# Performance work log

Hardware: AMD Instinct MI355X
Metric: run time of the kernel (lower is better)

Reference implementation:

```python
import jax, jax.numpy as jnp
import numpy as np

E = 1024
M = 6
GH = 256
FR = 16  # FiLM bottleneck r = max(16, E//64)


def setup_inputs() -> dict:
    key = jax.random.key(0)
    ks = jax.random.split(key, 32)
    n = lambda k, shape, std=0.02: jax.random.normal(k, shape, dtype=jnp.float32) * std
    inp = {
        "x": jax.random.normal(ks[0], (4, 2048, E), dtype=jnp.float32),
        # gate MLP E->GH->M
        "gw1": n(ks[1], (E, GH)), "gb1": jnp.zeros((GH,), jnp.float32),
        "gw2": n(ks[2], (GH, M)), "gb2": jnp.zeros((M,), jnp.float32),
        "ebias": jnp.zeros((M,), jnp.float32),
        "pm_alpha": jnp.float32(0.5),
        # expert 0: DoubleMLP E->2E->E
        "dfc_w": n(ks[3], (E, 2 * E)), "dfc_b": jnp.zeros((2 * E,), jnp.float32),
        "dproj_w": n(ks[4], (2 * E, E)), "dproj_b": jnp.zeros((E,), jnp.float32),
        # expert 1: SingleMLP E->E->E
        "sfc_w": n(ks[5], (E, E)), "sfc_b": jnp.zeros((E,), jnp.float32),
        "sproj_w": n(ks[6], (E, E)), "sproj_b": jnp.zeros((E,), jnp.float32),
        # expert 2: rank-2 perceptron
        "p2_w": n(ks[7], (2, E)), "p2_v": n(ks[8], (2, E)),
        "p2_alpha": jnp.ones((2,), jnp.float32), "p2_b": jnp.zeros((2,), jnp.float32),
        "p2_bias": jnp.zeros((E,), jnp.float32),
        # expert 3: rank-4 perceptron
        "p4_w": n(ks[9], (4, E)), "p4_v": n(ks[10], (4, E)),
        "p4_alpha": jnp.ones((4,), jnp.float32), "p4_b": jnp.zeros((4,), jnp.float32),
        "p4_bias": jnp.zeros((E,), jnp.float32),
        # expert 4: ReGLU1D
        "rg_u": n(ks[11], (E,)), "rg_a": jnp.ones((E,), jnp.float32),
        "rg_b": jnp.zeros((1,), jnp.float32), "rg_bias": jnp.zeros((E,), jnp.float32),
        # expert 5: FiLM E->FR->2E
        "fl_dw": n(ks[12], (E, FR)), "fl_db": jnp.zeros((FR,), jnp.float32),
        "fl_uw": n(ks[13], (FR, 2 * E)), "fl_ub": jnp.zeros((2 * E,), jnp.float32),
    }
    return inp


def _gelu(x):
    return jax.nn.gelu(x, approximate=False)  # torch nn.GELU default (erf)


def _rank_n(x, w, v, alpha, b, biasvec):
    # y = biasvec + sum_i alpha_i * gelu(<w_i,x> + b_i) * v_i
    s = jnp.einsum("bse,ne->bsn", x, w) + b
    g = _gelu(s)
    return jnp.einsum("bsn,ne->bse", alpha * g, v) + biasvec


def reference(x, gw1, gb1, gw2, gb2, ebias, pm_alpha,
              dfc_w, dfc_b, dproj_w, dproj_b,
              sfc_w, sfc_b, sproj_w, sproj_b,
              p2_w, p2_v, p2_alpha, p2_b, p2_bias,
              p4_w, p4_v, p4_alpha, p4_b, p4_bias,
              rg_u, rg_a, rg_b, rg_bias,
              fl_dw, fl_db, fl_uw, fl_ub):
    # gate logits [B,S,M]; tau=1.0
    gl = _gelu(x @ gw1 + gb1) @ gw2 + gb2 + ebias
    pi = jax.nn.softmax(gl, axis=-1)
    # top_k=1 sparse weights: mask to top-1 then renormalize
    _, topi = jax.lax.top_k(pi, 1)
    mask = jax.nn.one_hot(topi[..., 0], M, dtype=pi.dtype)
    w = pi * mask
    w = w / (jnp.sum(w, axis=-1, keepdims=True) + 1e-9)

    # experts (dropout = identity in eval)
    o0 = _gelu(x @ dfc_w + dfc_b) @ dproj_w + dproj_b            # DoubleMLP
    o1 = _gelu(x @ sfc_w + sfc_b) @ sproj_w + sproj_b            # SingleMLP
    o2 = _rank_n(x, p2_w, p2_v, p2_alpha, p2_b, p2_bias)          # perc2
    o3 = _rank_n(x, p4_w, p4_v, p4_alpha, p4_b, p4_bias)          # perc4
    s = x @ rg_u + rg_b[0]                                        # ReGLU1D
    o4 = jax.nn.sigmoid(s)[..., None] * (x * rg_a) + rg_bias
    t = _gelu(x @ fl_dw + fl_db)                                  # FiLM
    gb = t @ fl_uw + fl_ub
    gamma, beta = jnp.split(gb, 2, axis=-1)
    o5 = gamma * x + beta

    all_out = jnp.stack([o0, o1, o2, o3, o4, o5], axis=-1)        # [B,S,E,M]
    mixed = jnp.sum(all_out * w[..., None, :], axis=-1)
    return pm_alpha * mixed
```

## Files before the change

### kernel.cpp

```cpp
#include <hip/hip_runtime.h>
#include <math.h>


#define E 1024
#define GH 256
#define NEXP 6
#define NTOK 8192
#define NCH 24

typedef __attribute__((ext_vector_type(8))) short bf16x8;
typedef __attribute__((ext_vector_type(4))) float f32x4;

__device__ __forceinline__ float gelu_erf(float v) {
    return 0.5f * v * (1.0f + erff(v * 0.70710678118654752440f));
}

__device__ __forceinline__ unsigned short f2bf(float f) {
    union { float f; unsigned u; } c; c.f = f;
    unsigned u = c.u;
    u += 0x7fffu + ((u >> 16) & 1u);
    return (unsigned short)(u >> 16);
}

__device__ __forceinline__ float bf2f(unsigned short h) {
    union { unsigned u; float f; } c; c.u = ((unsigned)h) << 16;
    return c.f;
}

__device__ __forceinline__ int ldso(int row, int q) {
    return row * 32 + ((q ^ ((row >> 1) & 3)) << 3);
}

__device__ __forceinline__ void glds16(const void* g, void* l) {
    __builtin_amdgcn_global_load_lds(
        (const __attribute__((address_space(1))) void*)g,
        (__attribute__((address_space(3))) void*)l, 16, 0, 0);
}

__global__ __launch_bounds__(256)
void prep_kernel(const float* __restrict__ x, unsigned short* __restrict__ xh,
                 unsigned short* __restrict__ xl,
                 const float* __restrict__ gw1, unsigned short* __restrict__ w1cat,
                 const float* __restrict__ p2_w, const float* __restrict__ p4_w,
                 const float* __restrict__ rg_u, const float* __restrict__ fl_dw,
                 unsigned short* __restrict__ w1cheap,
                 const float* __restrict__ dfc_w, unsigned short* __restrict__ dfc_wt,
                 const float* __restrict__ dproj_w, unsigned short* __restrict__ dpj_wt,
                 const float* __restrict__ sfc_w, unsigned short* __restrict__ sfc_wt,
                 const float* __restrict__ sproj_w, unsigned short* __restrict__ spj_wt) {
    __shared__ float tile[32][33];
    const int tid = threadIdx.x;
    const int tx = tid & 31, ty = tid >> 5;
    int b = blockIdx.x;
    if (b < 2048) {
        const int n4 = NTOK * E / 4;
        for (int i = b * 256 + tid; i < n4; i += 2048 * 256) {
            float4 v = reinterpret_cast<const float4*>(x)[i];
            ushort4 h, l;
            h.x = f2bf(v.x); l.x = f2bf(v.x - bf2f(h.x));
            h.y = f2bf(v.y); l.y = f2bf(v.y - bf2f(h.y));
            h.z = f2bf(v.z); l.z = f2bf(v.z - bf2f(h.z));
            h.w = f2bf(v.w); l.w = f2bf(v.w - bf2f(h.w));
            reinterpret_cast<ushort4*>(xh)[i] = h;
            reinterpret_cast<ushort4*>(xl)[i] = l;
        }
        return;
    }
    b -= 2048;
    if (b < 256) {
        const int c0 = (b & 7) * 32, r0 = (b >> 3) * 32;
#pragma unroll
        for (int i = 0; i < 4; ++i)
            tile[ty + i * 8][tx] = gw1[(size_t)(r0 + ty + i * 8) * GH + c0 + tx];
        __syncthreads();
#pragma unroll
        for (int i = 0; i < 4; ++i) {
            float v = tile[tx][ty + i * 8];
            unsigned short h = f2bf(v);
            size_t row = (size_t)(c0 + ty + i * 8) * 2048;
            w1cat[row + r0 + tx] = h;
            w1cat[row + 1024 + r0 + tx] = f2bf(v - bf2f(h));
        }
        return;
    }
    b -= 256;
    if (b < 64) {
        const int r = b;
        const int k4 = tid * 4;
        float4 v = {0.f, 0.f, 0.f, 0.f};
        if (r < 2)       v = *reinterpret_cast<const float4*>(&p2_w[r * E + k4]);
        else if (r < 6)  v = *reinterpret_cast<const float4*>(&p4_w[(r - 2) * E + k4]);
        else if (r == 6) v = *reinterpret_cast<const float4*>(&rg_u[k4]);
        else if (r < 23) {
            const int j = r - 7;
            v.x = fl_dw[(k4 + 0) * 16 + j];
            v.y = fl_dw[(k4 + 1) * 16 + j];
            v.z = fl_dw[(k4 + 2) * 16 + j];
            v.w = fl_dw[(k4 + 3) * 16 + j];
        }
        ushort4 h, l;
        h.x = f2bf(v.x); l.x = f2bf(v.x - bf2f(h.x));
        h.y = f2bf(v.y); l.y = f2bf(v.y - bf2f(h.y));
        h.z = f2bf(v.z); l.z = f2bf(v.z - bf2f(h.z));
        h.w = f2bf(v.w); l.w = f2bf(v.w - bf2f(h.w));
        *reinterpret_cast<ushort4*>(&w1cheap[r * 2048 + k4]) = h;
        *reinterpret_cast<ushort4*>(&w1cheap[r * 2048 + 1024 + k4]) = l;
        return;
    }
    b -= 64;
    const float* src; unsigned short* dst; int R, C, nbx;
    if (b < 2048)      { src = dfc_w;   dst = dfc_wt; R = 1024; C = 2048; nbx = 64; }
    else if (b < 4096) { src = dproj_w; dst = dpj_wt; R = 2048; C = 1024; nbx = 32; b -= 2048; }
    else if (b < 5120) { src = sfc_w;   dst = sfc_wt; R = 1024; C = 1024; nbx = 32; b -= 4096; }
    else               { src = sproj_w; dst = spj_wt; R = 1024; C = 1024; nbx = 32; b -= 5120; }
    const int c0 = (b % nbx) * 32, r0 = (b / nbx) * 32;
#pragma unroll
    for (int i = 0; i < 4; ++i)
        tile[ty + i * 8][tx] = src[(size_t)(r0 + ty + i * 8) * C + c0 + tx];
    __syncthreads();
#pragma unroll
    for (int i = 0; i < 4; ++i)
        dst[(size_t)(c0 + ty + i * 8) * R + r0 + tx] = f2bf(tile[tx][ty + i * 8]);
}

__global__ __launch_bounds__(256)
void gate_partial_kernel(const unsigned short* __restrict__ xh,
                         const unsigned short* __restrict__ xl,
                         const unsigned short* __restrict__ w1cat,
                         const unsigned short* __restrict__ w1cheap,
                         float* __restrict__ hp,
                         float* __restrict__ cdot) {
    __shared__ __align__(16) unsigned short As[2][128 * 32];
    __shared__ __align__(16) unsigned short Bs[2][128 * 32];
    const int tid = threadIdx.x;
    const int bid = blockIdx.x;
    const int xcd = bid & 7, slot = bid >> 3;
    const int nx = slot & 1;
    const int strip = xcd * 32 + (slot >> 1);
    const int m = strip >> 2, c2 = strip & 3;
    const int z = c2 & 1, h = c2 >> 1;
    const int t0 = m * 128, n0 = nx * 128;
    const unsigned short* A = z ? xl : xh;
    float* hpz = hp + (size_t)c2 * ((size_t)NTOK * GH);
    float* cd  = cdot + (size_t)c2 * ((size_t)NTOK * NCH);

    const int lane = tid & 63, wv = tid >> 6;
    const int wr = wv >> 1, wc = wv & 1;
    const int lm = lane & 15, q = lane >> 4;
    const int r0 = tid >> 2, gsl = tid & 3;
    const int g = gsl ^ ((r0 >> 1) & 3);
    const int lbase = wv * 512;

    const unsigned short* pa0 = A + (size_t)(t0 + r0) * E + g * 8;
    const unsigned short* pa1 = A + (size_t)(t0 + 64 + r0) * E + g * 8;
    const unsigned short* pb0 = w1cat + (size_t)(n0 + r0) * 2048 + h * 1024 + g * 8;
    const unsigned short* pb1 = w1cat + (size_t)(n0 + 64 + r0) * 2048 + h * 1024 + g * 8;
    const unsigned short* pcw = w1cheap + (size_t)(nx * 16 + lm) * 2048 + h * 1024 + q * 8;

    f32x4 acc[4][4];
#pragma unroll
    for (int s = 0; s < 4; ++s)
#pragma unroll
        for (int t = 0; t < 4; ++t) acc[s][t] = (f32x4){0.f, 0.f, 0.f, 0.f};
    f32x4 accC[2];
    accC[0] = (f32x4){0.f, 0.f, 0.f, 0.f};
    accC[1] = (f32x4){0.f, 0.f, 0.f, 0.f};

    glds16(pa0, &As[0][lbase]);
    glds16(pa1, &As[0][2048 + lbase]);
    glds16(pb0, &Bs[0][lbase]);
    glds16(pb1, &Bs[0][2048 + lbase]);
    bf16x8 cfv = *(const bf16x8*)pcw;

    int cur = 0;
    for (int k0 = 0;; k0 += 32) {
        __syncthreads();
        const int kn = k0 + 32;
        bf16x8 cfn;
        if (kn < 1024) {
            glds16(pa0 + kn, &As[cur ^ 1][lbase]);
            glds16(pa1 + kn, &As[cur ^ 1][2048 + lbase]);
            glds16(pb0 + kn, &Bs[cur ^ 1][lbase]);
            glds16(pb1 + kn, &Bs[cur ^ 1][2048 + lbase]);
            cfn = *(const bf16x8*)(pcw + kn);
        }
        bf16x8 af[4], bfr[4];
#pragma unroll
        for (int s = 0; s < 4; ++s) af[s] = *(const bf16x8*)&As[cur][ldso(wr * 64 + s * 16 + lm, q)];
#pragma unroll
        for (int t = 0; t < 4; ++t) bfr[t] = *(const bf16x8*)&Bs[cur][ldso(wc * 64 + t * 16 + lm, q)];
#pragma unroll
        for (int s = 0; s < 4; ++s)
#pragma unroll
            for (int t = 0; t < 4; ++t)
                acc[s][t] = __builtin_amdgcn_mfma_f32_16x16x32_bf16(af[s], bfr[t], acc[s][t], 0, 0, 0);
        {
            bf16x8 ac0 = wc ? af[2] : af[0];
            bf16x8 ac1 = wc ? af[3] : af[1];
            accC[0] = __builtin_amdgcn_mfma_f32_16x16x32_bf16(ac0, cfv, accC[0], 0, 0, 0);
            accC[1] = __builtin_amdgcn_mfma_f32_16x16x32_bf16(ac1, cfv, accC[1], 0, 0, 0);
        }
        if (kn >= 1024) break;
        cfv = cfn; cur ^= 1;
    }
#pragma unroll
    for (int s = 0; s < 4; ++s)
#pragma unroll
        for (int t = 0; t < 4; ++t)
#pragma unroll
            for (int rg = 0; rg < 4; ++rg) {
                int rl = wr * 64 + s * 16 + q * 4 + rg;
                int c  = wc * 64 + t * 16 + lm;
                hpz[(size_t)(t0 + rl) * GH + n0 + c] = acc[s][t][rg];
            }
    const int cc = nx * 16 + lm;
    if (cc < NCH) {
#pragma unroll
        for (int i = 0; i < 2; ++i)
#pragma unroll
            for (int rg = 0; rg < 4; ++rg) {
                int rl = wr * 64 + wc * 32 + i * 16 + q * 4 + rg;
                cd[(size_t)(t0 + rl) * NCH + cc] = accC[i][rg];
            }
    }
}

__global__ __launch_bounds__(256)
void gate_finalize_kernel(const float* __restrict__ hp,
                          const float* __restrict__ gb1, const float* __restrict__ gw2,
                          const float* __restrict__ gb2, const float* __restrict__ ebias,
                          const float* __restrict__ pm_alpha,
                          const float* __restrict__ cdot,
                          const float* __restrict__ p2_alpha, const float* __restrict__ p2_b,
                          const float* __restrict__ p4_alpha, const float* __restrict__ p4_b,
                          const float* __restrict__ rg_b, const float* __restrict__ fl_db,
                          float* __restrict__ scale, int* __restrict__ counts,
                          int* __restrict__ tlist, int* __restrict__ eid,
                          float* __restrict__ gvec) {
    __shared__ float hs[32][264];
    __shared__ float g2s[GH * NEXP];
    __shared__ int tokexp[32];
    const int tid = threadIdx.x;
    const int t0 = blockIdx.x * 32;
    const size_t HPS = (size_t)NTOK * GH;
    for (int i = tid; i < GH * NEXP; i += 256) g2s[i] = gw2[i];
#pragma unroll
    for (int i = 0; i < 8; ++i) {
        int f4 = i * 256 + tid;
        int row = f4 >> 6, c4 = (f4 & 63) * 4;
        size_t base = (size_t)(t0 + row) * GH + c4;
        float4 a = *reinterpret_cast<const float4*>(&hp[base]);
        float4 b = *reinterpret_cast<const float4*>(&hp[HPS + base]);
        float4 c = *reinterpret_cast<const float4*>(&hp[2 * HPS + base]);
        float4 d = *reinterpret_cast<const float4*>(&hp[3 * HPS + base]);
        float4 o;
        o.x = gelu_erf(a.x + b.x + c.x + d.x + gb1[c4 + 0]);
        o.y = gelu_erf(a.y + b.y + c.y + d.y + gb1[c4 + 1]);
        o.z = gelu_erf(a.z + b.z + c.z + d.z + gb1[c4 + 2]);
        o.w = gelu_erf(a.w + b.w + c.w + d.w + gb1[c4 + 3]);
        *reinterpret_cast<float4*>(&hs[row][c4]) = o;
    }
    __syncthreads();
    const int t = tid >> 3, j = tid & 7;
    float p[NEXP] = {0.f, 0.f, 0.f, 0.f, 0.f, 0.f};
#pragma unroll 8
    for (int kk = 0; kk < 32; ++kk) {
        int k = j + kk * 8;
        float hv = hs[t][k];
        const float* gr = &g2s[k * NEXP];
#pragma unroll
        for (int m = 0; m < NEXP; ++m) p[m] += hv * gr[m];
    }
#pragma unroll
    for (int m = 0; m < NEXP; ++m) {
        p[m] += __shfl_xor(p[m], 4, 64);
        p[m] += __shfl_xor(p[m], 2, 64);
        p[m] += __shfl_xor(p[m], 1, 64);
    }
    if (j == 0) {
        float L[NEXP];
#pragma unroll
        for (int m = 0; m < NEXP; ++m) L[m] = p[m] + gb2[m] + ebias[m];
        float mx = L[0]; int am = 0;
#pragma unroll
        for (int m = 1; m < NEXP; ++m) { if (L[m] > mx) { mx = L[m]; am = m; } }
        float S = 0.f;
#pragma unroll
        for (int m = 0; m < NEXP; ++m) S += expf(L[m] - mx);
        float pt = 1.f / S;
        scale[t0 + t] = pm_alpha[0] * (pt / (pt + 1e-9f));
        eid[t0 + t] = am;
        tokexp[t] = am;
    }
    __syncthreads();
    if (tid < NEXP) {
        const int e = tid;
        int cnt = 0;
#pragma unroll
        for (int i = 0; i < 32; ++i) cnt += (tokexp[i] == e);
        if (cnt) {
            int base = atomicAdd(&counts[e], cnt);
            int pos = 0;
#pragma unroll
            for (int i = 0; i < 32; ++i)
                if (tokexp[i] == e) tlist[e * NTOK + base + (pos++)] = t0 + i;
        }
    }
    const size_t CDS = (size_t)NTOK * NCH;
    for (int i = tid; i < 32 * NCH; i += 256) {
        const int tt = i / NCH, slot = i - tt * NCH;
        const int tok = t0 + tt;
        size_t idx = (size_t)tok * NCH + slot;
        float s = cdot[idx] + cdot[CDS + idx] + cdot[2 * CDS + idx] + cdot[3 * CDS + idx];
        float val;
        if (slot < 2)       val = p2_alpha[slot] * gelu_erf(s + p2_b[slot]);
        else if (slot < 6)  val = p4_alpha[slot - 2] * gelu_erf(s + p4_b[slot - 2]);
        else if (slot == 6) val = 1.f / (1.f + expf(-(s + rg_b[0])));
        else if (slot < 23) val = gelu_erf(s + fl_db[slot - 7]);
        else                val = 0.f;
        gvec[(size_t)tok * NCH + slot] = val;
    }
}

__global__ __launch_bounds__(256)
void moe_gemm1_kernel(const unsigned short* __restrict__ xh,
                      const unsigned short* __restrict__ B0, const unsigned short* __restrict__ B1,
                      const float* __restrict__ bias0, const float* __restrict__ bias1,
                      const int* __restrict__ counts, const int* __restrict__ tlist,
                      unsigned short* __restrict__ H0, unsigned short* __restrict__ H1) {
    __shared__ __align__(16) unsigned short As[2][64 * 32];
    __shared__ __align__(16) unsigned short Bs[2][64 * 32];
    __shared__ int toks[64];
    const int tid = threadIdx.x;
    const int bid = blockIdx.x;
    const int xcd = bid & 7, slot = bid >> 3;
    const int nx = slot & 31;
    const int strip = xcd + 8 * (slot >> 5);
    const int z = strip & 1;
    const int N = z ? 1024 : 2048;
    const int cnt = counts[z];
    const int i0 = (strip >> 1) * 64;
    const int n0 = nx * 64;
    if (i0 >= cnt || n0 >= N) return;
    const unsigned short* Bz = z ? B1 : B0;
    const float* bias = z ? bias1 : bias0;

    if (tid < 64) toks[tid] = tlist[z * NTOK + min(i0 + tid, cnt - 1)];
    __syncthreads();

    const int lane = tid & 63, wv = tid >> 6;
    const int wm = (wv & 1) * 32, wn = (wv >> 1) * 32;
    const int lm = lane & 15, q = lane >> 4;
    const int r0 = tid >> 2, gsl = tid & 3;
    const int g = gsl ^ ((r0 >> 1) & 3);
    const int lbase = wv * 512;

    const unsigned short* pa = xh + (size_t)toks[r0] * E + g * 8;
    const unsigned short* pb = Bz + (size_t)(n0 + r0) * E + g * 8;

    f32x4 acc[2][2];
#pragma unroll
    for (int s = 0; s < 2; ++s)
#pragma unroll
        for (int t = 0; t < 2; ++t) acc[s][t] = (f32x4){0.f, 0.f, 0.f, 0.f};

    glds16(pa, &As[0][lbase]);
    glds16(pb, &Bs[0][lbase]);

    int cur = 0;
    for (int k0 = 0;; k0 += 32) {
        __syncthreads();
        const int kn = k0 + 32;
        if (kn < E) {
            glds16(pa + kn, &As[cur ^ 1][lbase]);
            glds16(pb + kn, &Bs[cur ^ 1][lbase]);
        }
        bf16x8 af[2], bfr[2];
#pragma unroll
        for (int s = 0; s < 2; ++s) af[s] = *(const bf16x8*)&As[cur][ldso(wm + s * 16 + lm, q)];
#pragma unroll
        for (int t = 0; t < 2; ++t) bfr[t] = *(const bf16x8*)&Bs[cur][ldso(wn + t * 16 + lm, q)];
#pragma unroll
        for (int s = 0; s < 2; ++s)
#pragma unroll
            for (int t = 0; t < 2; ++t)
                acc[s][t] = __builtin_amdgcn_mfma_f32_16x16x32_bf16(af[s], bfr[t], acc[s][t], 0, 0, 0);
        if (kn >= E) break;
        cur ^= 1;
    }
    unsigned short* Hz = z ? H1 : H0;
#pragma unroll
    for (int s = 0; s < 2; ++s)
#pragma unroll
        for (int t = 0; t < 2; ++t)
#pragma unroll
            for (int rg = 0; rg < 4; ++rg) {
                int rl = wm + s * 16 + q * 4 + rg;
                int gc = n0 + wn + t * 16 + lm;
                float v = acc[s][t][rg] + bias[gc];
                Hz[(size_t)(i0 + rl) * N + gc] = f2bf(gelu_erf(v));
            }
}

__global__ __launch_bounds__(256)
void gemm2_cheap_kernel(const unsigned short* __restrict__ h1, const unsigned short* __restrict__ h2,
                        const unsigned short* __restrict__ dpj, const unsigned short* __restrict__ spj,
                        const float* __restrict__ dproj_b, const float* __restrict__ sproj_b,
                        const int* __restrict__ counts, const int* __restrict__ tlist,
                        const float* __restrict__ scale,
                        const float* __restrict__ x, const float* __restrict__ gvec,
                        const float* __restrict__ p2_v, const float* __restrict__ p2_bias,
                        const float* __restrict__ p4_v, const float* __restrict__ p4_bias,
                        const float* __restrict__ rg_a, const float* __restrict__ rg_bias,
                        const float* __restrict__ fl_uw, const float* __restrict__ fl_ub,
                        float* __restrict__ out) {
    __shared__ __align__(16) char smem[2 * 64 * 32 * 2 * 2 + 64 * 4];
    const int tid = threadIdx.x;
    const int bb = blockIdx.x;
    const int lane = tid & 63;

    if (bb < 1024) {
        const int xcd = bb & 7, slot = bb >> 3;
        const int nx = slot & 15;
        const int strip = xcd + 8 * (slot >> 4);
        const int z = strip & 1;
        const int i0 = (strip >> 1) * 64;
        const int n0 = nx * 64;
        const int K = z ? 1024 : 2048;
        const int cnt = counts[z];
        if (i0 >= cnt) return;
        const int rows = min(64, cnt - i0);
        const unsigned short* Az = z ? h2 : h1;
        const unsigned short* Bz = z ? spj : dpj;
        const float* bias = z ? sproj_b : dproj_b;

        unsigned short (*As)[64 * 32] = (unsigned short (*)[64 * 32])smem;
        unsigned short (*Bs)[64 * 32] = (unsigned short (*)[64 * 32])(smem + 2 * 64 * 32 * 2);
        int* toks = (int*)(smem + 2 * 64 * 32 * 2 * 2);
        if (tid < 64) toks[tid] = tlist[z * NTOK + min(i0 + tid, cnt - 1)];
        __syncthreads();

        const int wv = tid >> 6;
        const int wm = (wv & 1) * 32, wn = (wv >> 1) * 32;
        const int lm = lane & 15, q = lane >> 4;
        const int r0 = tid >> 2, gsl = tid & 3;
        const int g = gsl ^ ((r0 >> 1) & 3);
        const int lbase = wv * 512;

        const unsigned short* pa = Az + (size_t)(i0 + r0) * K + g * 8;
        const unsigned short* pb = Bz + (size_t)(n0 + r0) * K + g * 8;

        f32x4 acc[2][2];
#pragma unroll
        for (int s = 0; s < 2; ++s)
#pragma unroll
            for (int t = 0; t < 2; ++t) acc[s][t] = (f32x4){0.f, 0.f, 0.f, 0.f};

        glds16(pa, &As[0][lbase]);
        glds16(pb, &Bs[0][lbase]);

        int cur = 0;
        for (int k0 = 0;; k0 += 32) {
            __syncthreads();
            const int kn = k0 + 32;
            if (kn < K) {
                glds16(pa + kn, &As[cur ^ 1][lbase]);
                glds16(pb + kn, &Bs[cur ^ 1][lbase]);
            }
            bf16x8 af[2], bfr[2];
#pragma unroll
            for (int s = 0; s < 2; ++s) af[s] = *(const bf16x8*)&As[cur][ldso(wm + s * 16 + lm, q)];
#pragma unroll
            for (int t = 0; t < 2; ++t) bfr[t] = *(const bf16x8*)&Bs[cur][ldso(wn + t * 16 + lm, q)];
#pragma unroll
            for (int s = 0; s < 2; ++s)
#pragma unroll
                for (int t = 0; t < 2; ++t)
                    acc[s][t] = __builtin_amdgcn_mfma_f32_16x16x32_bf16(af[s], bfr[t], acc[s][t], 0, 0, 0);
            if (kn >= K) break;
            cur ^= 1;
        }
#pragma unroll
        for (int s = 0; s < 2; ++s)
#pragma unroll
            for (int t = 0; t < 2; ++t)
#pragma unroll
                for (int rg = 0; rg < 4; ++rg) {
                    int rl = wm + s * 16 + q * 4 + rg;
                    if (rl < rows) {
                        int gc = n0 + wn + t * 16 + lm;
                        int tok = toks[rl];
                        out[(size_t)tok * E + gc] = scale[tok] * (acc[s][t][rg] + bias[gc]);
                    }
                }
        return;
    }

    int* stoks = (int*)smem;
    float* ssc = (float*)(smem + 32);
    float (*sgv)[17] = (float (*)[17])(smem + 64);
    const int k4 = tid * 4;
    for (int s = bb - 1024; s < 4096; s += 2048) {
        const int e = 2 + (s & 3);
        const int ti = s >> 2;
        const int cnt = counts[e];
        const int i0 = ti * 8;
        if (i0 >= cnt) continue;
        const int nt = min(8, cnt - i0);
        __syncthreads();
        if (tid < 128) {
            const int tt = tid >> 4, sl = tid & 15;
            const int tk = tlist[e * NTOK + min(i0 + tt, cnt - 1)];
            if (sl == 0) { stoks[tt] = tk; ssc[tt] = scale[tk]; }
            const int base = (e == 2) ? 0 : (e == 3) ? 2 : (e == 4) ? 6 : 7;
            const int ng   = (e == 2) ? 2 : (e == 3) ? 4 : (e == 4) ? 1 : 16;
            if (sl < ng) sgv[tt][sl] = gvec[(size_t)tk * NCH + base + sl];
        }
        __syncthreads();
        if (e == 2) {
            const float4 b0 = *reinterpret_cast<const float4*>(&p2_bias[k4]);
            const float4 v0 = *reinterpret_cast<const float4*>(&p2_v[k4]);
            const float4 v1 = *reinterpret_cast<const float4*>(&p2_v[E + k4]);
#pragma unroll
            for (int tt = 0; tt < 8; ++tt) {
                if (tt < nt) {
                    const float g0 = sgv[tt][0], g1 = sgv[tt][1], sc = ssc[tt];
                    float4 o;
                    o.x = (b0.x + g0 * v0.x + g1 * v1.x) * sc;
                    o.y = (b0.y + g0 * v0.y + g1 * v1.y) * sc;
                    o.z = (b0.z + g0 * v0.z + g1 * v1.z) * sc;
                    o.w = (b0.w + g0 * v0.w + g1 * v1.w) * sc;
                    *reinterpret_cast<float4*>(&out[(size_t)stoks[tt] * E + k4]) = o;
                }
            }
        } else if (e == 3) {
            const float4 b0 = *reinterpret_cast<const float4*>(&p4_bias[k4]);
            float4 vv[4];
#pragma unroll
            for (int j = 0; j < 4; ++j)
                vv[j] = *reinterpret_cast<const float4*>(&p4_v[j * E + k4]);
#pragma unroll
            for (int tt = 0; tt < 8; ++tt) {
                if (tt < nt) {
                    float4 o = b0;
#pragma unroll
                    for (int j = 0; j < 4; ++j) {
                        const float gj = sgv[tt][j];
                        o.x += gj * vv[j].x; o.y += gj * vv[j].y;
                        o.z += gj * vv[j].z; o.w += gj * vv[j].w;
                    }
                    const float sc = ssc[tt];
                    o.x *= sc; o.y *= sc; o.z *= sc; o.w *= sc;
                    *reinterpret_cast<float4*>(&out[(size_t)stoks[tt] * E + k4]) = o;
                }
            }
        } else if (e == 4) {
            const float4 av = *reinterpret_cast<const float4*>(&rg_a[k4]);
            const float4 bv = *reinterpret_cast<const float4*>(&rg_bias[k4]);
#pragma unroll
            for (int tt = 0; tt < 8; ++tt) {
                if (tt < nt) {
                    const float sg = sgv[tt][0], sc = ssc[tt];
                    const float4 xv = *reinterpret_cast<const float4*>(&x[(size_t)stoks[tt] * E + k4]);
                    float4 o;
                    o.x = (sg * xv.x * av.x + bv.x) * sc;
                    o.y = (sg * xv.y * av.y + bv.y) * sc;
                    o.z = (sg * xv.z * av.z + bv.z) * sc;
                    o.w = (sg * xv.w * av.w + bv.w) * sc;
                    *reinterpret_cast<float4*>(&out[(size_t)stoks[tt] * E + k4]) = o;
                }
            }
        } else {
            float4 ga[8], be[8];
            const float4 g0 = *reinterpret_cast<const float4*>(&fl_ub[k4]);
            const float4 b0 = *reinterpret_cast<const float4*>(&fl_ub[E + k4]);
#pragma unroll
            for (int tt = 0; tt < 8; ++tt) { ga[tt] = g0; be[tt] = b0; }
#pragma unroll
            for (int j = 0; j < 16; ++j) {
                const float4 ug = *reinterpret_cast<const float4*>(&fl_uw[(size_t)j * 2 * E + k4]);
                const float4 ub = *reinterpret_cast<const float4*>(&fl_uw[(size_t)j * 2 * E + E + k4]);
#pragma unroll
                for (int tt = 0; tt < 8; ++tt) {
                    const float tj = sgv[tt][j];
                    ga[tt].x += tj * ug.x; ga[tt].y += tj * ug.y;
                    ga[tt].z += tj * ug.z; ga[tt].w += tj * ug.w;
                    be[tt].x += tj * ub.x; be[tt].y += tj * ub.y;
                    be[tt].z += tj * ub.z; be[tt].w += tj * ub.w;
                }
            }
#pragma unroll
            for (int tt = 0; tt < 8; ++tt) {
                if (tt < nt) {
                    const float sc = ssc[tt];
                    const float4 xv = *reinterpret_cast<const float4*>(&x[(size_t)stoks[tt] * E + k4]);
                    float4 o;
                    o.x = (ga[tt].x * xv.x + be[tt].x) * sc;
                    o.y = (ga[tt].y * xv.y + be[tt].y) * sc;
                    o.z = (ga[tt].z * xv.z + be[tt].z) * sc;
                    o.w = (ga[tt].w * xv.w + be[tt].w) * sc;
                    *reinterpret_cast<float4*>(&out[(size_t)stoks[tt] * E + k4]) = o;
                }
            }
        }
    }
}

extern "C" void kernel_launch(void* const* d_in, const int* in_sizes, int n_in,
                              void* d_out, int out_size, void* d_ws, size_t ws_size,
                              hipStream_t stream) {
    const float* x        = (const float*)d_in[0];
    const float* gw1      = (const float*)d_in[1];
    const float* gb1      = (const float*)d_in[2];
    const float* gw2      = (const float*)d_in[3];
    const float* gb2      = (const float*)d_in[4];
    const float* ebias    = (const float*)d_in[5];
    const float* pm_alpha = (const float*)d_in[6];
    const float* dfc_w    = (const float*)d_in[7];
    const float* dfc_b    = (const float*)d_in[8];
    const float* dproj_w  = (const float*)d_in[9];
    const float* dproj_b  = (const float*)d_in[10];
    const float* sfc_w    = (const float*)d_in[11];
    const float* sfc_b    = (const float*)d_in[12];
    const float* sproj_w  = (const float*)d_in[13];
    const float* sproj_b  = (const float*)d_in[14];
    const float* p2_w     = (const float*)d_in[15];
    const float* p2_v     = (const float*)d_in[16];
    const float* p2_alpha = (const float*)d_in[17];
    const float* p2_b     = (const float*)d_in[18];
    const float* p2_bias  = (const float*)d_in[19];
    const float* p4_w     = (const float*)d_in[20];
    const float* p4_v     = (const float*)d_in[21];
    const float* p4_alpha = (const float*)d_in[22];
    const float* p4_b     = (const float*)d_in[23];
    const float* p4_bias  = (const float*)d_in[24];
    const float* rg_u     = (const float*)d_in[25];
    const float* rg_a     = (const float*)d_in[26];
    const float* rg_b     = (const float*)d_in[27];
    const float* rg_bias  = (const float*)d_in[28];
    const float* fl_dw    = (const float*)d_in[29];
    const float* fl_db    = (const float*)d_in[30];
    const float* fl_uw    = (const float*)d_in[31];
    const float* fl_ub    = (const float*)d_in[32];
    float* out = (float*)d_out;

    char* ws = (char*)d_ws;
    size_t off = 0;
    int*            counts = (int*)(ws + off);            off += 256;
    float*          scale  = (float*)(ws + off);          off += (size_t)NTOK * 4;
    int*            tlist  = (int*)(ws + off);            off += (size_t)NEXP * NTOK * 4;
    int*            eid    = (int*)(ws + off);            off += (size_t)NTOK * 4;
    float*          gvec   = (float*)(ws + off);          off += (size_t)NTOK * NCH * 4;
    float*          cdot   = (float*)(ws + off);          off += (size_t)4 * NTOK * NCH * 4;
    unsigned short* w1cheap= (unsigned short*)(ws + off); off += (size_t)64 * 2048 * 2;
    unsigned short* w1cat  = (unsigned short*)(ws + off); off += (size_t)GH * 2048 * 2;
    unsigned short* dfc_wt = (unsigned short*)(ws + off); off += (size_t)2048 * 1024 * 2;
    unsigned short* dpj_wt = (unsigned short*)(ws + off); off += (size_t)1024 * 2048 * 2;
    unsigned short* sfc_wt = (unsigned short*)(ws + off); off += (size_t)1024 * 1024 * 2;
    unsigned short* spj_wt = (unsigned short*)(ws + off); off += (size_t)1024 * 1024 * 2;
    unsigned short* x_hi   = (unsigned short*)(ws + off); off += (size_t)NTOK * E * 2;
    char* U = ws + off;
    unsigned short* x_lo = (unsigned short*)U;
    unsigned short* h1   = (unsigned short*)U;
    unsigned short* h2   = (unsigned short*)(U + (size_t)16 * 1024 * 1024);
    float* hp = out;

    hipMemsetAsync(counts, 0, 256, stream);
    prep_kernel<<<8512, 256, 0, stream>>>(x, x_hi, x_lo, gw1, w1cat,
                                          p2_w, p4_w, rg_u, fl_dw, w1cheap,
                                          dfc_w, dfc_wt, dproj_w, dpj_wt,
                                          sfc_w, sfc_wt, sproj_w, spj_wt);
    gate_partial_kernel<<<512, 256, 0, stream>>>(
        x_hi, x_lo, w1cat, w1cheap, hp, cdot);
    gate_finalize_kernel<<<NTOK / 32, 256, 0, stream>>>(
        hp, gb1, gw2, gb2, ebias, pm_alpha, cdot,
        p2_alpha, p2_b, p4_alpha, p4_b, rg_b, fl_db,
        scale, counts, tlist, eid, gvec);
    moe_gemm1_kernel<<<2048, 256, 0, stream>>>(
        x_hi, dfc_wt, sfc_wt, dfc_b, sfc_b, counts, tlist, h1, h2);
    gemm2_cheap_kernel<<<1024 + 2048, 256, 0, stream>>>(
        h1, h2, dpj_wt, spj_wt, dproj_b, sproj_b, counts, tlist, scale,
        x, gvec,
        p2_v, p2_bias, p4_v, p4_bias,
        rg_a, rg_bias, fl_uw, fl_ub, out);
    (void)in_sizes; (void)n_in; (void)out_size; (void)ws_size;
}
```

Measured before the change: 294.0 us.

## Fuse cheap experts into gemm1 launch and double K-step per iteration

The cheap-expert blocks (perceptrons, ReGLU, FiLM) now ride alongside the first MoE GEMM instead of the second, and the second GEMM becomes its own kernel. All bf16 GEMM loops (gate, gemm1, gemm2) now stage 64-wide K tiles per barrier instead of 32, halving the number of syncs. The FiLM path is split into two halves of four tokens to reduce register pressure. The larger LDS footprint may lower occupancy.

```diff
diff --git a/kernel.cpp b/kernel.cpp
--- a/kernel.cpp
+++ b/kernel.cpp
@@ -130,8 +130,8 @@
                          const unsigned short* __restrict__ w1cheap,
                          float* __restrict__ hp,
                          float* __restrict__ cdot) {
-    __shared__ __align__(16) unsigned short As[2][128 * 32];
-    __shared__ __align__(16) unsigned short Bs[2][128 * 32];
+    __shared__ __align__(16) unsigned short As[2][128 * 64];
+    __shared__ __align__(16) unsigned short Bs[2][128 * 64];
     const int tid = threadIdx.x;
     const int bid = blockIdx.x;
     const int xcd = bid & 7, slot = bid >> 3;
@@ -168,40 +168,53 @@
 
     glds16(pa0, &As[0][lbase]);
     glds16(pa1, &As[0][2048 + lbase]);
+    glds16(pa0 + 32, &As[0][4096 + lbase]);
+    glds16(pa1 + 32, &As[0][4096 + 2048 + lbase]);
     glds16(pb0, &Bs[0][lbase]);
     glds16(pb1, &Bs[0][2048 + lbase]);
-    bf16x8 cfv = *(const bf16x8*)pcw;
+    glds16(pb0 + 32, &Bs[0][4096 + lbase]);
+    glds16(pb1 + 32, &Bs[0][4096 + 2048 + lbase]);
+    bf16x8 cf0 = *(const bf16x8*)pcw;
+    bf16x8 cf1 = *(const bf16x8*)(pcw + 32);
 
     int cur = 0;
-    for (int k0 = 0;; k0 += 32) {
+    for (int k0 = 0;; k0 += 64) {
         __syncthreads();
-        const int kn = k0 + 32;
-        bf16x8 cfn;
+        const int kn = k0 + 64;
+        bf16x8 cf0n, cf1n;
         if (kn < 1024) {
             glds16(pa0 + kn, &As[cur ^ 1][lbase]);
             glds16(pa1 + kn, &As[cur ^ 1][2048 + lbase]);
+            glds16(pa0 + kn + 32, &As[cur ^ 1][4096 + lbase]);
+            glds16(pa1 + kn + 32, &As[cur ^ 1][4096 + 2048 + lbase]);
             glds16(pb0 + kn, &Bs[cur ^ 1][lbase]);
             glds16(pb1 + kn, &Bs[cur ^ 1][2048 + lbase]);
-            cfn = *(const bf16x8*)(pcw + kn);
-        }
-        bf16x8 af[4], bfr[4];
-#pragma unroll
-        for (int s = 0; s < 4; ++s) af[s] = *(const bf16x8*)&As[cur][ldso(wr * 64 + s * 16 + lm, q)];
-#pragma unroll
-        for (int t = 0; t < 4; ++t) bfr[t] = *(const bf16x8*)&Bs[cur][ldso(wc * 64 + t * 16 + lm, q)];
-#pragma unroll
-        for (int s = 0; s < 4; ++s)
-#pragma unroll
-            for (int t = 0; t < 4; ++t)
-                acc[s][t] = __builtin_amdgcn_mfma_f32_16x16x32_bf16(af[s], bfr[t], acc[s][t], 0, 0, 0);
-        {
+            glds16(pb0 + kn + 32, &Bs[cur ^ 1][4096 + lbase]);
+            glds16(pb1 + kn + 32, &Bs[cur ^ 1][4096 + 2048 + lbase]);
+            cf0n = *(const bf16x8*)(pcw + kn);
+            cf1n = *(const bf16x8*)(pcw + kn + 32);
+        }
+#pragma unroll
+        for (int sub = 0; sub < 2; ++sub) {
+            const int off = sub * 4096;
+            bf16x8 af[4], bfr[4];
+#pragma unroll
+            for (int s = 0; s < 4; ++s) af[s] = *(const bf16x8*)&As[cur][off + ldso(wr * 64 + s * 16 + lm, q)];
+#pragma unroll
+            for (int t = 0; t < 4; ++t) bfr[t] = *(const bf16x8*)&Bs[cur][off + ldso(wc * 64 + t * 16 + lm, q)];
+#pragma unroll
+            for (int s = 0; s < 4; ++s)
+#pragma unroll
+                for (int t = 0; t < 4; ++t)
+                    acc[s][t] = __builtin_amdgcn_mfma_f32_16x16x32_bf16(af[s], bfr[t], acc[s][t], 0, 0, 0);
+            bf16x8 cf = sub ? cf1 : cf0;
             bf16x8 ac0 = wc ? af[2] : af[0];
             bf16x8 ac1 = wc ? af[3] : af[1];
-            accC[0] = __builtin_amdgcn_mfma_f32_16x16x32_bf16(ac0, cfv, accC[0], 0, 0, 0);
-            accC[1] = __builtin_amdgcn_mfma_f32_16x16x32_bf16(ac1, cfv, accC[1], 0, 0, 0);
+            accC[0] = __builtin_amdgcn_mfma_f32_16x16x32_bf16(ac0, cf, accC[0], 0, 0, 0);
+            accC[1] = __builtin_amdgcn_mfma_f32_16x16x32_bf16(ac1, cf, accC[1], 0, 0, 0);
         }
         if (kn >= 1024) break;
-        cfv = cfn; cur ^= 1;
+        cf0 = cf0n; cf1 = cf1n; cur ^= 1;
     }
 #pragma unroll
     for (int s = 0; s < 4; ++s)
@@ -323,120 +336,39 @@
 }
 
 __global__ __launch_bounds__(256)
-void moe_gemm1_kernel(const unsigned short* __restrict__ xh,
-                      const unsigned short* __restrict__ B0, const unsigned short* __restrict__ B1,
-                      const float* __restrict__ bias0, const float* __restrict__ bias1,
-                      const int* __restrict__ counts, const int* __restrict__ tlist,
-                      unsigned short* __restrict__ H0, unsigned short* __restrict__ H1) {
-    __shared__ __align__(16) unsigned short As[2][64 * 32];
-    __shared__ __align__(16) unsigned short Bs[2][64 * 32];
-    __shared__ int toks[64];
-    const int tid = threadIdx.x;
-    const int bid = blockIdx.x;
-    const int xcd = bid & 7, slot = bid >> 3;
-    const int nx = slot & 31;
-    const int strip = xcd + 8 * (slot >> 5);
-    const int z = strip & 1;
-    const int N = z ? 1024 : 2048;
-    const int cnt = counts[z];
-    const int i0 = (strip >> 1) * 64;
-    const int n0 = nx * 64;
-    if (i0 >= cnt || n0 >= N) return;
-    const unsigned short* Bz = z ? B1 : B0;
-    const float* bias = z ? bias1 : bias0;
-
-    if (tid < 64) toks[tid] = tlist[z * NTOK + min(i0 + tid, cnt - 1)];
-    __syncthreads();
-
-    const int lane = tid & 63, wv = tid >> 6;
-    const int wm = (wv & 1) * 32, wn = (wv >> 1) * 32;
-    const int lm = lane & 15, q = lane >> 4;
-    const int r0 = tid >> 2, gsl = tid & 3;
-    const int g = gsl ^ ((r0 >> 1) & 3);
-    const int lbase = wv * 512;
-
-    const unsigned short* pa = xh + (size_t)toks[r0] * E + g * 8;
-    const unsigned short* pb = Bz + (size_t)(n0 + r0) * E + g * 8;
-
-    f32x4 acc[2][2];
-#pragma unroll
-    for (int s = 0; s < 2; ++s)
-#pragma unroll
-        for (int t = 0; t < 2; ++t) acc[s][t] = (f32x4){0.f, 0.f, 0.f, 0.f};
-
-    glds16(pa, &As[0][lbase]);
-    glds16(pb, &Bs[0][lbase]);
-
-    int cur = 0;
-    for (int k0 = 0;; k0 += 32) {
-        __syncthreads();
-        const int kn = k0 + 32;
-        if (kn < E) {
-            glds16(pa + kn, &As[cur ^ 1][lbase]);
-            glds16(pb + kn, &Bs[cur ^ 1][lbase]);
-        }
-        bf16x8 af[2], bfr[2];
-#pragma unroll
-        for (int s = 0; s < 2; ++s) af[s] = *(const bf16x8*)&As[cur][ldso(wm + s * 16 + lm, q)];
-#pragma unroll
-        for (int t = 0; t < 2; ++t) bfr[t] = *(const bf16x8*)&Bs[cur][ldso(wn + t * 16 + lm, q)];
-#pragma unroll
-        for (int s = 0; s < 2; ++s)
-#pragma unroll
-            for (int t = 0; t < 2; ++t)
-                acc[s][t] = __builtin_amdgcn_mfma_f32_16x16x32_bf16(af[s], bfr[t], acc[s][t], 0, 0, 0);
-        if (kn >= E) break;
-        cur ^= 1;
-    }
-    unsigned short* Hz = z ? H1 : H0;
-#pragma unroll
-    for (int s = 0; s < 2; ++s)
-#pragma unroll
-        for (int t = 0; t < 2; ++t)
-#pragma unroll
-            for (int rg = 0; rg < 4; ++rg) {
-                int rl = wm + s * 16 + q * 4 + rg;
-                int gc = n0 + wn + t * 16 + lm;
-                float v = acc[s][t][rg] + bias[gc];
-                Hz[(size_t)(i0 + rl) * N + gc] = f2bf(gelu_erf(v));
-            }
-}
-
-__global__ __launch_bounds__(256)
-void gemm2_cheap_kernel(const unsigned short* __restrict__ h1, const unsigned short* __restrict__ h2,
-                        const unsigned short* __restrict__ dpj, const unsigned short* __restrict__ spj,
-                        const float* __restrict__ dproj_b, const float* __restrict__ sproj_b,
+void gemm1_cheap_kernel(const unsigned short* __restrict__ xh,
+                        const unsigned short* __restrict__ B0, const unsigned short* __restrict__ B1,
+                        const float* __restrict__ bias0, const float* __restrict__ bias1,
                         const int* __restrict__ counts, const int* __restrict__ tlist,
-                        const float* __restrict__ scale,
-                        const float* __restrict__ x, const float* __restrict__ gvec,
+                        unsigned short* __restrict__ H0, unsigned short* __restrict__ H1,
+                        const float* __restrict__ scale, const float* __restrict__ x,
+                        const float* __restrict__ gvec,
                         const float* __restrict__ p2_v, const float* __restrict__ p2_bias,
                         const float* __restrict__ p4_v, const float* __restrict__ p4_bias,
                         const float* __restrict__ rg_a, const float* __restrict__ rg_bias,
                         const float* __restrict__ fl_uw, const float* __restrict__ fl_ub,
                         float* __restrict__ out) {
-    __shared__ __align__(16) char smem[2 * 64 * 32 * 2 * 2 + 64 * 4];
+    __shared__ __align__(16) char smem[2 * 64 * 64 * 2 * 2 + 64 * 4];
     const int tid = threadIdx.x;
     const int bb = blockIdx.x;
     const int lane = tid & 63;
 
-    if (bb < 1024) {
+    if (bb < 2048) {
         const int xcd = bb & 7, slot = bb >> 3;
-        const int nx = slot & 15;
-        const int strip = xcd + 8 * (slot >> 4);
+        const int nx = slot & 31;
+        const int strip = xcd + 8 * (slot >> 5);
         const int z = strip & 1;
+        const int N = z ? 1024 : 2048;
+        const int cnt = counts[z];
         const int i0 = (strip >> 1) * 64;
         const int n0 = nx * 64;
-        const int K = z ? 1024 : 2048;
-        const int cnt = counts[z];
-        if (i0 >= cnt) return;
-        const int rows = min(64, cnt - i0);
-        const unsigned short* Az = z ? h2 : h1;
-        const unsigned short* Bz = z ? spj : dpj;
-        const float* bias = z ? sproj_b : dproj_b;
-
-        unsigned short (*As)[64 * 32] = (unsigned short (*)[64 * 32])smem;
-        unsigned short (*Bs)[64 * 32] = (unsigned short (*)[64 * 32])(smem + 2 * 64 * 32 * 2);
-        int* toks = (int*)(smem + 2 * 64 * 32 * 2 * 2);
+        if (i0 >= cnt || n0 >= N) return;
+        const unsigned short* Bz = z ? B1 : B0;
+        const float* bias = z ? bias1 : bias0;
+
+        unsigned short (*As)[64 * 64] = (unsigned short (*)[64 * 64])smem;
+        unsigned short (*Bs)[64 * 64] = (unsigned short (*)[64 * 64])(smem + 2 * 64 * 64 * 2);
+        int* toks = (int*)(smem + 2 * 64 * 64 * 2 * 2);
         if (tid < 64) toks[tid] = tlist[z * NTOK + min(i0 + tid, cnt - 1)];
         __syncthreads();
 
@@ -447,8 +379,8 @@
         const int g = gsl ^ ((r0 >> 1) & 3);
         const int lbase = wv * 512;
 
-        const unsigned short* pa = Az + (size_t)(i0 + r0) * K + g * 8;
-        const unsigned short* pb = Bz + (size_t)(n0 + r0) * K + g * 8;
+        const unsigned short* pa = xh + (size_t)toks[r0] * E + g * 8;
+        const unsigned short* pb = Bz + (size_t)(n0 + r0) * E + g * 8;
 
         f32x4 acc[2][2];
 #pragma unroll
@@ -457,29 +389,38 @@
             for (int t = 0; t < 2; ++t) acc[s][t] = (f32x4){0.f, 0.f, 0.f, 0.f};
 
         glds16(pa, &As[0][lbase]);
+        glds16(pa + 32, &As[0][2048 + lbase]);
         glds16(pb, &Bs[0][lbase]);
+        glds16(pb + 32, &Bs[0][2048 + lbase]);
 
         int cur = 0;
-        for (int k0 = 0;; k0 += 32) {
+        for (int k0 = 0;; k0 += 64) {
             __syncthreads();
-            const int kn = k0 + 32;
-            if (kn < K) {
+            const int kn = k0 + 64;
+            if (kn < E) {
                 glds16(pa + kn, &As[cur ^ 1][lbase]);
+                glds16(pa + kn + 32, &As[cur ^ 1][2048 + lbase]);
                 glds16(pb + kn, &Bs[cur ^ 1][lbase]);
-            }
-            bf16x8 af[2], bfr[2];
-#pragma unroll
-            for (int s = 0; s < 2; ++s) af[s] = *(const bf16x8*)&As[cur][ldso(wm + s * 16 + lm, q)];
-#pragma unroll
-            for (int t = 0; t < 2; ++t) bfr[t] = *(const bf16x8*)&Bs[cur][ldso(wn + t * 16 + lm, q)];
-#pragma unroll
-            for (int s = 0; s < 2; ++s)
-#pragma unroll
-                for (int t = 0; t < 2; ++t)
-                    acc[s][t] = __builtin_amdgcn_mfma_f32_16x16x32_bf16(af[s], bfr[t], acc[s][t], 0, 0, 0);
-            if (kn >= K) break;
+                glds16(pb + kn + 32, &Bs[cur ^ 1][2048 + lbase]);
+            }
+#pragma unroll
+            for (int sub = 0; sub < 2; ++sub) {
+                const int off = sub * 2048;
+                bf16x8 af[2], bfr[2];
+#pragma unroll
+                for (int s = 0; s < 2; ++s) af[s] = *(const bf16x8*)&As[cur][off + ldso(wm + s * 16 + lm, q)];
+#pragma unroll
+                for (int t = 0; t < 2; ++t) bfr[t] = *(const bf16x8*)&Bs[cur][off + ldso(wn + t * 16 + lm, q)];
+#pragma unroll
+                for (int s = 0; s < 2; ++s)
+#pragma unroll
+                    for (int t = 0; t < 2; ++t)
+                        acc[s][t] = __builtin_amdgcn_mfma_f32_16x16x32_bf16(af[s], bfr[t], acc[s][t], 0, 0, 0);
+            }
+            if (kn >= E) break;
             cur ^= 1;
         }
+        unsigned short* Hz = z ? H1 : H0;
 #pragma unroll
         for (int s = 0; s < 2; ++s)
 #pragma unroll
@@ -487,11 +428,9 @@
 #pragma unroll
                 for (int rg = 0; rg < 4; ++rg) {
                     int rl = wm + s * 16 + q * 4 + rg;
-                    if (rl < rows) {
-                        int gc = n0 + wn + t * 16 + lm;
-                        int tok = toks[rl];
-                        out[(size_t)tok * E + gc] = scale[tok] * (acc[s][t][rg] + bias[gc]);
-                    }
+                    int gc = n0 + wn + t * 16 + lm;
+                    float v = acc[s][t][rg] + bias[gc];
+                    Hz[(size_t)(i0 + rl) * N + gc] = f2bf(gelu_erf(v));
                 }
         return;
     }
@@ -500,7 +439,7 @@
     float* ssc = (float*)(smem + 32);
     float (*sgv)[17] = (float (*)[17])(smem + 64);
     const int k4 = tid * 4;
-    for (int s = bb - 1024; s < 4096; s += 2048) {
+    for (int s = bb - 2048; s < 4096; s += 2048) {
         const int e = 2 + (s & 3);
         const int ti = s >> 2;
         const int cnt = counts[e];
@@ -571,39 +510,137 @@
                 }
             }
         } else {
-            float4 ga[8], be[8];
-            const float4 g0 = *reinterpret_cast<const float4*>(&fl_ub[k4]);
-            const float4 b0 = *reinterpret_cast<const float4*>(&fl_ub[E + k4]);
-#pragma unroll
-            for (int tt = 0; tt < 8; ++tt) { ga[tt] = g0; be[tt] = b0; }
-#pragma unroll
-            for (int j = 0; j < 16; ++j) {
-                const float4 ug = *reinterpret_cast<const float4*>(&fl_uw[(size_t)j * 2 * E + k4]);
-                const float4 ub = *reinterpret_cast<const float4*>(&fl_uw[(size_t)j * 2 * E + E + k4]);
-#pragma unroll
-                for (int tt = 0; tt < 8; ++tt) {
-                    const float tj = sgv[tt][j];
-                    ga[tt].x += tj * ug.x; ga[tt].y += tj * ug.y;
-                    ga[tt].z += tj * ug.z; ga[tt].w += tj * ug.w;
-                    be[tt].x += tj * ub.x; be[tt].y += tj * ub.y;
-                    be[tt].z += tj * ub.z; be[tt].w += tj * ub.w;
+#pragma unroll
+            for (int half = 0; half < 2; ++half) {
+                float4 ga[4], be[4];
+                const float4 g0 = *reinterpret_cast<const float4*>(&fl_ub[k4]);
+                const float4 b0 = *reinterpret_cast<const float4*>(&fl_ub[E + k4]);
+#pragma unroll
+                for (int tt = 0; tt < 4; ++tt) { ga[tt] = g0; be[tt] = b0; }
+#pragma unroll
+                for (int j = 0; j < 16; ++j) {
+                    const float4 ug = *reinterpret_cast<const float4*>(&fl_uw[(size_t)j * 2 * E + k4]);
+                    const float4 ub = *reinterpret_cast<const float4*>(&fl_uw[(size_t)j * 2 * E + E + k4]);
+#pragma unroll
+                    for (int tt = 0; tt < 4; ++tt) {
+                        const float tj = sgv[half * 4 + tt][j];
+                        ga[tt].x += tj * ug.x; ga[tt].y += tj * ug.y;
+                        ga[tt].z += tj * ug.z; ga[tt].w += tj * ug.w;
+                        be[tt].x += tj * ub.x; be[tt].y += tj * ub.y;
+                        be[tt].z += tj * ub.z; be[tt].w += tj * ub.w;
+                    }
                 }
-            }
-#pragma unroll
-            for (int tt = 0; tt < 8; ++tt) {
-                if (tt < nt) {
-                    const float sc = ssc[tt];
-                    const float4 xv = *reinterpret_cast<const float4*>(&x[(size_t)stoks[tt] * E + k4]);
-                    float4 o;
-                    o.x = (ga[tt].x * xv.x + be[tt].x) * sc;
-                    o.y = (ga[tt].y * xv.y + be[tt].y) * sc;
-                    o.z = (ga[tt].z * xv.z + be[tt].z) * sc;
-                    o.w = (ga[tt].w * xv.w + be[tt].w) * sc;
-                    *reinterpret_cast<float4*>(&out[(size_t)stoks[tt] * E + k4]) = o;
+#pragma unroll
+                for (int tt = 0; tt < 4; ++tt) {
+                    const int ix = half * 4 + tt;
+                    if (ix < nt) {
+                        const float sc = ssc[ix];
+                        const float4 xv = *reinterpret_cast<const float4*>(&x[(size_t)stoks[ix] * E + k4]);
+                        float4 o;
+                        o.x = (ga[tt].x * xv.x + be[tt].x) * sc;
+                        o.y = (ga[tt].y * xv.y + be[tt].y) * sc;
+                        o.z = (ga[tt].z * xv.z + be[tt].z) * sc;
+                        o.w = (ga[tt].w * xv.w + be[tt].w) * sc;
+                        *reinterpret_cast<float4*>(&out[(size_t)stoks[ix] * E + k4]) = o;
+                    }
                 }
             }
         }
     }
+}
+
+__global__ __launch_bounds__(256)
+void moe_gemm2_kernel(const unsigned short* __restrict__ h1, const unsigned short* __restrict__ h2,
+                      const unsigned short* __restrict__ dpj, const unsigned short* __restrict__ spj,
+                      const float* __restrict__ dproj_b, const float* __restrict__ sproj_b,
+                      const int* __restrict__ counts, const int* __restrict__ tlist,
+                      const float* __restrict__ scale,
+                      float* __restrict__ out) {
+    __shared__ __align__(16) unsigned short As[2][64 * 64];
+    __shared__ __align__(16) unsigned short Bs[2][64 * 64];
+    __shared__ int toks[64];
+    const int tid = threadIdx.x;
+    const int bb = blockIdx.x;
+    const int lane = tid & 63;
+
+    const int xcd = bb & 7, slot = bb >> 3;
+    const int nx = slot & 15;
+    const int strip = xcd + 8 * (slot >> 4);
+    const int z = strip & 1;
+    const int i0 = (strip >> 1) * 64;
+    const int n0 = nx * 64;
+    const int K = z ? 1024 : 2048;
+    const int cnt = counts[z];
+    if (i0 >= cnt) return;
+    const int rows = min(64, cnt - i0);
+    const unsigned short* Az = z ? h2 : h1;
+    const unsigned short* Bz = z ? spj : dpj;
+    const float* bias = z ? sproj_b : dproj_b;
+
+    if (tid < 64) toks[tid] = tlist[z * NTOK + min(i0 + tid, cnt - 1)];
+    __syncthreads();
+
+    const int wv = tid >> 6;
+    const int wm = (wv & 1) * 32, wn = (wv >> 1) * 32;
+    const int lm = lane & 15, q = lane >> 4;
+    const int r0 = tid >> 2, gsl = tid & 3;
+    const int g = gsl ^ ((r0 >> 1) & 3);
+    const int lbase = wv * 512;
+
+    const unsigned short* pa = Az + (size_t)(i0 + r0) * K + g * 8;
+    const unsigned short* pb = Bz + (size_t)(n0 + r0) * K + g * 8;
+
+    f32x4 acc[2][2];
+#pragma unroll
+    for (int s = 0; s < 2; ++s)
+#pragma unroll
+        for (int t = 0; t < 2; ++t) acc[s][t] = (f32x4){0.f, 0.f, 0.f, 0.f};
+
+    glds16(pa, &As[0][lbase]);
+    glds16(pa + 32, &As[0][2048 + lbase]);
+    glds16(pb, &Bs[0][lbase]);
+    glds16(pb + 32, &Bs[0][2048 + lbase]);
+
+    int cur = 0;
+    for (int k0 = 0;; k0 += 64) {
+        __syncthreads();
+        const int kn = k0 + 64;
+        if (kn < K) {
+            glds16(pa + kn, &As[cur ^ 1][lbase]);
+            glds16(pa + kn + 32, &As[cur ^ 1][2048 + lbase]);
+            glds16(pb + kn, &Bs[cur ^ 1][lbase]);
+            glds16(pb + kn + 32, &Bs[cur ^ 1][2048 + lbase]);
+        }
+#pragma unroll
+        for (int sub = 0; sub < 2; ++sub) {
+            const int off = sub * 2048;
+            bf16x8 af[2], bfr[2];
+#pragma unroll
+            for (int s = 0; s < 2; ++s) af[s] = *(const bf16x8*)&As[cur][off + ldso(wm + s * 16 + lm, q)];
+#pragma unroll
+            for (int t = 0; t < 2; ++t) bfr[t] = *(const bf16x8*)&Bs[cur][off + ldso(wn + t * 16 + lm, q)];
+#pragma unroll
+            for (int s = 0; s < 2; ++s)
+#pragma unroll
+                for (int t = 0; t < 2; ++t)
+                    acc[s][t] = __builtin_amdgcn_mfma_f32_16x16x32_bf16(af[s], bfr[t], acc[s][t], 0, 0, 0);
+        }
+        if (kn >= K) break;
+        cur ^= 1;
+    }
+#pragma unroll
+    for (int s = 0; s < 2; ++s)
+#pragma unroll
+        for (int t = 0; t < 2; ++t)
+#pragma unroll
+            for (int rg = 0; rg < 4; ++rg) {
+                int rl = wm + s * 16 + q * 4 + rg;
+                if (rl < rows) {
+                    int gc = n0 + wn + t * 16 + lm;
+                    int tok = toks[rl];
+                    out[(size_t)tok * E + gc] = scale[tok] * (acc[s][t][rg] + bias[gc]);
+                }
+            }
 }
 
 extern "C" void kernel_launch(void* const* d_in, const int* in_sizes, int n_in,
@@ -676,12 +713,12 @@
         hp, gb1, gw2, gb2, ebias, pm_alpha, cdot,
         p2_alpha, p2_b, p4_alpha, p4_b, rg_b, fl_db,
         scale, counts, tlist, eid, gvec);
-    moe_gemm1_kernel<<<2048, 256, 0, stream>>>(
-        x_hi, dfc_wt, sfc_wt, dfc_b, sfc_b, counts, tlist, h1, h2);
-    gemm2_cheap_kernel<<<1024 + 2048, 256, 0, stream>>>(
-        h1, h2, dpj_wt, spj_wt, dproj_b, sproj_b, counts, tlist, scale,
-        x, gvec,
+    gemm1_cheap_kernel<<<4096, 256, 0, stream>>>(
+        x_hi, dfc_wt, sfc_wt, dfc_b, sfc_b, counts, tlist, h1, h2,
+        scale, x, gvec,
         p2_v, p2_bias, p4_v, p4_bias,
         rg_a, rg_bias, fl_uw, fl_ub, out);
+    moe_gemm2_kernel<<<1024, 256, 0, stream>>>(
+        h1, h2, dpj_wt, spj_wt, dproj_b, sproj_b, counts, tlist, scale, out);
     (void)in_sizes; (void)n_in; (void)out_size; (void)ws_size;
 }
```

Measured after the change: 291.1 us. No clear change (-1.0%).
